# Performance work log

Hardware: AMD Instinct MI355X
Metric: run time of the kernel (lower is better)

Reference implementation:

```python
import jax, jax.numpy as jnp
import numpy as np

B, T, E, H = 8, 2048, 1024, 64

def setup_inputs() -> dict:
    key = jax.random.key(0)
    k1, k2, k3, k4 = jax.random.split(key, 4)
    x = jax.random.normal(k1, (B, T, E), dtype=jnp.float32)
    # Linear(E, H, bias=False) weights stored as [E, H] (x @ W)
    s = 1.0 / np.sqrt(E)
    Wk = jax.random.normal(k2, (E, H), dtype=jnp.float32) * s
    Wq = jax.random.normal(k3, (E, H), dtype=jnp.float32) * s
    Wv = jax.random.normal(k4, (E, H), dtype=jnp.float32) * s
    return {"x": x, "Wk": Wk, "Wq": Wq, "Wv": Wv}

def reference(x, Wk, Wq, Wv):
    _, t, e = x.shape
    k = jnp.einsum('bte,eh->bth', x, Wk)
    q = jnp.einsum('bte,eh->bth', x, Wq)
    v = jnp.einsum('bte,eh->bth', x, Wv)
    # NOTE: original scales by E**-0.5 (embedding dim), not head_size**-0.5
    wei = jnp.einsum('bqh,bkh->bqk', q, k) * (e ** -0.5)
    causal = jnp.tril(jnp.ones((t, t), dtype=bool))
    wei = jnp.where(causal, wei, -jnp.inf)
    wei = jax.nn.softmax(wei, axis=-1)
    out = jnp.einsum('bqk,bkh->bqh', wei, v)
    return out
```

## Files before the change

### kernel.cpp

```cpp
#include <hip/hip_runtime.h>

typedef unsigned short u16;
typedef unsigned int u32;
typedef __bf16 bf16x8 __attribute__((ext_vector_type(8)));
typedef __bf16 bf16x4 __attribute__((ext_vector_type(4)));
typedef float f32x4 __attribute__((ext_vector_type(4)));

constexpr int Bn = 8, Tn = 2048, En = 1024, Hn = 64;
constexpr int Mrows = Bn * Tn;
constexpr float CEXP = 0.03125f * 1.4426950408889634f;

__device__ __forceinline__ u16 f2bf(float f) {
  u32 u = __float_as_uint(f);
  return (u16)((u + 0x7fffu + ((u >> 16) & 1u)) >> 16);
}

__global__ __launch_bounds__(256) void wt_kernel(
    const float* __restrict__ Wk, const float* __restrict__ Wq,
    const float* __restrict__ Wv, u16* __restrict__ Wt2) {
  __shared__ float tile[64][68];
  const int mat = blockIdx.x >> 4;
  const int tk = blockIdx.x & 15;
  const float* W = (mat == 0) ? Wk : (mat == 1) ? Wq : Wv;
  const int t = threadIdx.x;
#pragma unroll
  for (int i = 0; i < 4; ++i) {
    const int f = t + i * 256;
    const int el = f >> 4;
    const int h4 = f & 15;
    float4 v = *(const float4*)(W + (size_t)(tk * 64 + el) * Hn + h4 * 4);
    tile[el][h4 * 4 + 0] = v.x;
    tile[el][h4 * 4 + 1] = v.y;
    tile[el][h4 * 4 + 2] = v.z;
    tile[el][h4 * 4 + 3] = v.w;
  }
  __syncthreads();
#pragma unroll
  for (int c2 = 0; c2 < 2; ++c2) {
    const int c = t * 2 + c2;
    const int fi = c >> 6;
    const int l = c & 63;
    const int ht = fi >> 1, kss = fi & 1;
    const int q = l >> 4, l16 = l & 15;
    __align__(16) u16 buf[8];
#pragma unroll
    for (int j = 0; j < 8; ++j)
      buf[j] = f2bf(tile[kss * 32 + q * 8 + j][ht * 16 + l16]);
    u16* dst = Wt2 + ((size_t)(tk * 12 + mat * 4 + ht) * 2 + kss) * 512 + l * 8;
    *(uint4*)dst = *(const uint4*)buf;
  }
}

__global__ __launch_bounds__(256, 2) void qkv_kernel(
    const float* __restrict__ x, const u16* __restrict__ Wt2,
    u16* __restrict__ Kb16, u16* __restrict__ Qb16, u16* __restrict__ Vt16) {
  constexpr int NR = 32, BK = 128, LDK = BK + 8;
  __shared__ u16 xs[NR * LDK];
  const int t = threadIdx.x;
  const int w = t >> 6, lane = t & 63;
  const int quad = lane >> 4, l16 = lane & 15;
  const int r0 = blockIdx.x * NR;

  const int srow = t >> 5;
  const int scol = (t & 31) * 4;
  const float* xp = x + (size_t)(r0 + srow) * En + scol;
  u16* xsw0 = xs + srow * LDK + scol;

  const u16* wA = Wt2 + (size_t)lane * 8;

  f32x4 acc[3][2];
#pragma unroll
  for (int i = 0; i < 3; ++i)
#pragma unroll
    for (int nt = 0; nt < 2; ++nt) acc[i][nt] = (f32x4){0.f, 0.f, 0.f, 0.f};

  bf16x8 af[2][12];

#define LOADA(P, K0)                                                            \
  do {                                                                          \
    const int tb_ = ((K0) >> 6) * 12;                                           \
    _Pragma("unroll") for (int ks_ = 0; ks_ < 4; ++ks_)                         \
        _Pragma("unroll") for (int i_ = 0; i_ < 3; ++i_) {                      \
      const int frag_ = (tb_ + (ks_ >> 1) * 12 + (3 * w + i_)) * 2 + (ks_ & 1); \
      af[P][ks_ * 3 + i_] = *(const bf16x8*)(wA + (size_t)frag_ * 512);         \
    }                                                                           \
  } while (0)

  float4 pre[4];
#pragma unroll
  for (int i = 0; i < 4; ++i) pre[i] = *(const float4*)(xp + i * 8 * En);
  LOADA(0, 0);

#pragma unroll
  for (int s = 0; s < 8; ++s) {
    const int k0 = s * BK;
    const int par = s & 1;
    __syncthreads();
#pragma unroll
    for (int i = 0; i < 4; ++i) {
      bf16x4 pk;
      pk[0] = (__bf16)pre[i].x; pk[1] = (__bf16)pre[i].y;
      pk[2] = (__bf16)pre[i].z; pk[3] = (__bf16)pre[i].w;
      *(bf16x4*)(xsw0 + i * 8 * LDK) = pk;
    }
    __syncthreads();
    if (s < 7) {
#pragma unroll
      for (int i = 0; i < 4; ++i)
        pre[i] = *(const float4*)(xp + k0 + BK + i * 8 * En);
      LOADA(par ^ 1, k0 + BK);
    }
#pragma unroll
    for (int ks = 0; ks < 4; ++ks) {
      bf16x8 b0 = *(const bf16x8*)(xs + l16 * LDK + ks * 32 + quad * 8);
      bf16x8 b1 = *(const bf16x8*)(xs + (16 + l16) * LDK + ks * 32 + quad * 8);
#pragma unroll
      for (int i = 0; i < 3; ++i) {
        acc[i][0] = __builtin_amdgcn_mfma_f32_16x16x32_bf16(af[par][ks * 3 + i], b0, acc[i][0], 0, 0, 0);
        acc[i][1] = __builtin_amdgcn_mfma_f32_16x16x32_bf16(af[par][ks * 3 + i], b1, acc[i][1], 0, 0, 0);
      }
    }
  }
#undef LOADA

#pragma unroll
  for (int i = 0; i < 3; ++i) {
    const int mt = 3 * w + i;
    const int mat = mt >> 2, ht = mt & 3;
#pragma unroll
    for (int nt = 0; nt < 2; ++nt) {
      const int row = r0 + nt * 16 + l16;
      f32x4 a = acc[i][nt];
      if (mat < 2) {
        u16* dst = ((mat == 0) ? Kb16 : Qb16) + (size_t)row * Hn + ht * 16 + quad * 4;
        uint2 pk;
        pk.x = (u32)f2bf(a[0]) | ((u32)f2bf(a[1]) << 16);
        pk.y = (u32)f2bf(a[2]) | ((u32)f2bf(a[3]) << 16);
        *(uint2*)dst = pk;
      } else {
        const int bb = row >> 11, tt = row & 2047;
        u16* base = Vt16 + ((size_t)bb * 64) * Tn + tt;
#pragma unroll
        for (int r = 0; r < 4; ++r)
          base[(size_t)(ht * 16 + quad * 4 + r) * Tn] = f2bf(a[r]);
      }
    }
  }
}

__global__ __launch_bounds__(256, 2) void attn_kernel(
    const u16* __restrict__ Qb16, const u16* __restrict__ Kb16,
    const u16* __restrict__ Vt16, float* __restrict__ out) {
  __shared__ u16 pt[2][4][2][16][40];
  __shared__ float l_sh[2][4][16];
  __shared__ float o_sh[2][4][16][68];

  const int idx = blockIdx.x;
  const int b = idx & 7;
  const int tq = 63 - (idx >> 3);
  const int w = threadIdx.x >> 6, lane = threadIdx.x & 63;
  const int quad = lane >> 4, l16 = lane & 15;
  const int qbase = tq * 32;
  const int limit = qbase + 32;
  const int ch = ((limit + 127) >> 7) << 5;
  const int lo = w * ch;
  const int hi = min(lo + ch, limit);
  const int qa_abs = qbase + l16;
  const int qb_abs = qbase + 16 + l16;

  const u16* Kp = Kb16 + (size_t)b * Tn * Hn;
  const u16* Vp = Vt16 + (size_t)b * 64 * Tn;

  const u16* qrowA = Qb16 + ((size_t)b * Tn + qa_abs) * Hn + quad * 8;
  const u16* qrowB = qrowA + (size_t)16 * Hn;
  const bf16x8 qa0 = *(const bf16x8*)(qrowA);
  const bf16x8 qa1 = *(const bf16x8*)(qrowA + 32);
  const bf16x8 qb0 = *(const bf16x8*)(qrowB);
  const bf16x8 qb1 = *(const bf16x8*)(qrowB + 32);

  f32x4 oA0 = {0.f, 0.f, 0.f, 0.f}, oA1 = oA0, oA2 = oA0, oA3 = oA0;
  f32x4 oB0 = oA0, oB1 = oA0, oB2 = oA0, oB3 = oA0;
  f32x4 laccA = oA0, laccB = oA0;

#pragma unroll 2
  for (int kb = lo; kb < hi; kb += 32) {
    const int par = (kb >> 5) & 1;
    const u16* krow0 = Kp + (size_t)(kb + l16) * Hn + quad * 8;
    const u16* krow1 = krow0 + (size_t)16 * Hn;
    const bf16x8 k0lo = *(const bf16x8*)(krow0);
    const bf16x8 k0hi = *(const bf16x8*)(krow0 + 32);
    const bf16x8 k1lo = *(const bf16x8*)(krow1);
    const bf16x8 k1hi = *(const bf16x8*)(krow1 + 32);

    const f32x4 z = {0.f, 0.f, 0.f, 0.f};
    f32x4 s0a = __builtin_amdgcn_mfma_f32_16x16x32_bf16(k0lo, qa0, z, 0, 0, 0);
    s0a = __builtin_amdgcn_mfma_f32_16x16x32_bf16(k0hi, qa1, s0a, 0, 0, 0);
    f32x4 s1a = __builtin_amdgcn_mfma_f32_16x16x32_bf16(k1lo, qa0, z, 0, 0, 0);
    s1a = __builtin_amdgcn_mfma_f32_16x16x32_bf16(k1hi, qa1, s1a, 0, 0, 0);
    f32x4 s0b = __builtin_amdgcn_mfma_f32_16x16x32_bf16(k0lo, qb0, z, 0, 0, 0);
    s0b = __builtin_amdgcn_mfma_f32_16x16x32_bf16(k0hi, qb1, s0b, 0, 0, 0);
    f32x4 s1b = __builtin_amdgcn_mfma_f32_16x16x32_bf16(k1lo, qb0, z, 0, 0, 0);
    s1b = __builtin_amdgcn_mfma_f32_16x16x32_bf16(k1hi, qb1, s1b, 0, 0, 0);

    if (kb + 15 > qbase) {
#pragma unroll
      for (int r = 0; r < 4; ++r)
        if (kb + quad * 4 + r > qa_abs) s0a[r] = -3.0e38f;
    }
    if (kb + 31 > qbase) {
#pragma unroll
      for (int r = 0; r < 4; ++r)
        if (kb + 16 + quad * 4 + r > qa_abs) s1a[r] = -3.0e38f;
    }
    if (kb + 15 > qbase + 16) {
#pragma unroll
      for (int r = 0; r < 4; ++r)
        if (kb + quad * 4 + r > qb_abs) s0b[r] = -3.0e38f;
    }
    if (kb + 31 > qbase + 16) {
#pragma unroll
      for (int r = 0; r < 4; ++r)
        if (kb + 16 + quad * 4 + r > qb_abs) s1b[r] = -3.0e38f;
    }

    f32x4 pa0, pa1, pb0v, pb1v;
#pragma unroll
    for (int r = 0; r < 4; ++r) {
      pa0[r] = __builtin_amdgcn_exp2f(s0a[r] * CEXP);
      pa1[r] = __builtin_amdgcn_exp2f(s1a[r] * CEXP);
      pb0v[r] = __builtin_amdgcn_exp2f(s0b[r] * CEXP);
      pb1v[r] = __builtin_amdgcn_exp2f(s1b[r] * CEXP);
    }
    laccA += pa0;
    laccA += pa1;
    laccB += pb0v;
    laccB += pb1v;

    {
      bf16x4 wa0, wa1, wb0, wb1;
      wa0[0] = (__bf16)pa0[0]; wa0[1] = (__bf16)pa0[1];
      wa0[2] = (__bf16)pa0[2]; wa0[3] = (__bf16)pa0[3];
      wa1[0] = (__bf16)pa1[0]; wa1[1] = (__bf16)pa1[1];
      wa1[2] = (__bf16)pa1[2]; wa1[3] = (__bf16)pa1[3];
      wb0[0] = (__bf16)pb0v[0]; wb0[1] = (__bf16)pb0v[1];
      wb0[2] = (__bf16)pb0v[2]; wb0[3] = (__bf16)pb0v[3];
      wb1[0] = (__bf16)pb1v[0]; wb1[1] = (__bf16)pb1v[1];
      wb1[2] = (__bf16)pb1v[2]; wb1[3] = (__bf16)pb1v[3];
      *(bf16x4*)&pt[par][w][0][l16][quad * 4] = wa0;
      *(bf16x4*)&pt[par][w][0][l16][16 + quad * 4] = wa1;
      *(bf16x4*)&pt[par][w][1][l16][quad * 4] = wb0;
      *(bf16x4*)&pt[par][w][1][l16][16 + quad * 4] = wb1;
    }
    const bf16x8 pba = *(const bf16x8*)&pt[par][w][0][l16][quad * 8];
    const bf16x8 pbb = *(const bf16x8*)&pt[par][w][1][l16][quad * 8];

    const u16* vrow = Vp + (size_t)l16 * Tn + kb + quad * 8;
    const bf16x8 v0 = *(const bf16x8*)(vrow);
    const bf16x8 v1 = *(const bf16x8*)(vrow + (size_t)16 * Tn);
    const bf16x8 v2 = *(const bf16x8*)(vrow + (size_t)32 * Tn);
    const bf16x8 v3 = *(const bf16x8*)(vrow + (size_t)48 * Tn);

    oA0 = __builtin_amdgcn_mfma_f32_16x16x32_bf16(v0, pba, oA0, 0, 0, 0);
    oA1 = __builtin_amdgcn_mfma_f32_16x16x32_bf16(v1, pba, oA1, 0, 0, 0);
    oA2 = __builtin_amdgcn_mfma_f32_16x16x32_bf16(v2, pba, oA2, 0, 0, 0);
    oA3 = __builtin_amdgcn_mfma_f32_16x16x32_bf16(v3, pba, oA3, 0, 0, 0);
    oB0 = __builtin_amdgcn_mfma_f32_16x16x32_bf16(v0, pbb, oB0, 0, 0, 0);
    oB1 = __builtin_amdgcn_mfma_f32_16x16x32_bf16(v1, pbb, oB1, 0, 0, 0);
    oB2 = __builtin_amdgcn_mfma_f32_16x16x32_bf16(v2, pbb, oB2, 0, 0, 0);
    oB3 = __builtin_amdgcn_mfma_f32_16x16x32_bf16(v3, pbb, oB3, 0, 0, 0);
  }

  float la = (laccA[0] + laccA[1]) + (laccA[2] + laccA[3]);
  la += __shfl_xor(la, 16);
  la += __shfl_xor(la, 32);
  float lb = (laccB[0] + laccB[1]) + (laccB[2] + laccB[3]);
  lb += __shfl_xor(lb, 16);
  lb += __shfl_xor(lb, 32);
  if (quad == 0) {
    l_sh[0][w][l16] = la;
    l_sh[1][w][l16] = lb;
  }
  *(f32x4*)&o_sh[0][w][l16][0 * 16 + quad * 4] = oA0;
  *(f32x4*)&o_sh[0][w][l16][1 * 16 + quad * 4] = oA1;
  *(f32x4*)&o_sh[0][w][l16][2 * 16 + quad * 4] = oA2;
  *(f32x4*)&o_sh[0][w][l16][3 * 16 + quad * 4] = oA3;
  *(f32x4*)&o_sh[1][w][l16][0 * 16 + quad * 4] = oB0;
  *(f32x4*)&o_sh[1][w][l16][1 * 16 + quad * 4] = oB1;
  *(f32x4*)&o_sh[1][w][l16][2 * 16 + quad * 4] = oB2;
  *(f32x4*)&o_sh[1][w][l16][3 * 16 + quad * 4] = oB3;
  __syncthreads();

  const int qq = threadIdx.x >> 4, dq = threadIdx.x & 15;
#pragma unroll
  for (int tl = 0; tl < 2; ++tl) {
    float lg = 0.f;
    f32x4 acc = {0.f, 0.f, 0.f, 0.f};
#pragma unroll
    for (int ww = 0; ww < 4; ++ww) {
      lg += l_sh[tl][ww][qq];
      acc += *(const f32x4*)&o_sh[tl][ww][qq][dq * 4];
    }
    acc *= (1.f / lg);
    *(f32x4*)(out + ((size_t)b * Tn + qbase + tl * 16 + qq) * Hn + dq * 4) = acc;
  }
}

extern "C" void kernel_launch(void* const* d_in, const int* in_sizes, int n_in,
                              void* d_out, int out_size, void* d_ws, size_t ws_size,
                              hipStream_t stream) {
  const void* x = nullptr;
  const void* Ws[3] = {nullptr, nullptr, nullptr};
  int wj = 0;
  for (int i = 0; i < n_in; ++i) {
    if (in_sizes[i] == Bn * Tn * En) x = d_in[i];
    else if (wj < 3) Ws[wj++] = d_in[i];
  }
  const float* Wk = (const float*)Ws[0];
  const float* Wq = (const float*)Ws[1];
  const float* Wv = (const float*)Ws[2];

  u16* Kb16 = (u16*)d_ws;
  u16* Qb16 = Kb16 + (size_t)Mrows * Hn;
  u16* Vt16 = Qb16 + (size_t)Mrows * Hn;
  u16* Wt2  = Vt16 + (size_t)Mrows * Hn;

  wt_kernel<<<48, 256, 0, stream>>>(Wk, Wq, Wv, Wt2);
  qkv_kernel<<<Mrows / 32, 256, 0, stream>>>((const float*)x, Wt2, Kb16, Qb16, Vt16);
  attn_kernel<<<Bn * (Tn / 32), 256, 0, stream>>>(Qb16, Kb16, Vt16, (float*)d_out);
}
```

Before: 134.6 us.

## Split attention key range across eight waves per block with two-phase LDS reduction

New measurement: 134.8 us. Within noise of the previous version (+0.1%).

```diff
diff --git a/kernel.cpp b/kernel.cpp
--- a/kernel.cpp
+++ b/kernel.cpp
@@ -148,12 +148,14 @@
   }
 }
 
-__global__ __launch_bounds__(256, 2) void attn_kernel(
+__global__ __launch_bounds__(512, 4) void attn_kernel(
     const u16* __restrict__ Qb16, const u16* __restrict__ Kb16,
     const u16* __restrict__ Vt16, float* __restrict__ out) {
-  __shared__ u16 pt[2][4][2][16][40];
-  __shared__ float l_sh[2][4][16];
-  __shared__ float o_sh[2][4][16][68];
+  __shared__ __align__(16) char arena[34816];
+  __shared__ float l_sh[8][32];
+
+  u16* ptb = (u16*)arena;
+  float* osb = (float*)arena;
 
   const int idx = blockIdx.x;
   const int b = idx & 7;
@@ -162,7 +164,7 @@
   const int quad = lane >> 4, l16 = lane & 15;
   const int qbase = tq * 32;
   const int limit = qbase + 32;
-  const int ch = ((limit + 127) >> 7) << 5;
+  const int ch = ((limit + 255) >> 8) << 5;
   const int lo = w * ch;
   const int hi = min(lo + ch, limit);
   const int qa_abs = qbase + l16;
@@ -178,13 +180,14 @@
   const bf16x8 qb0 = *(const bf16x8*)(qrowB);
   const bf16x8 qb1 = *(const bf16x8*)(qrowB + 32);
 
+  u16* ptw = ptb + (size_t)w * (2 * 16 * 40);
+
   f32x4 oA0 = {0.f, 0.f, 0.f, 0.f}, oA1 = oA0, oA2 = oA0, oA3 = oA0;
   f32x4 oB0 = oA0, oB1 = oA0, oB2 = oA0, oB3 = oA0;
   f32x4 laccA = oA0, laccB = oA0;
 
 #pragma unroll 2
   for (int kb = lo; kb < hi; kb += 32) {
-    const int par = (kb >> 5) & 1;
     const u16* krow0 = Kp + (size_t)(kb + l16) * Hn + quad * 8;
     const u16* krow1 = krow0 + (size_t)16 * Hn;
     const bf16x8 k0lo = *(const bf16x8*)(krow0);
@@ -246,13 +249,13 @@
       wb0[2] = (__bf16)pb0v[2]; wb0[3] = (__bf16)pb0v[3];
       wb1[0] = (__bf16)pb1v[0]; wb1[1] = (__bf16)pb1v[1];
       wb1[2] = (__bf16)pb1v[2]; wb1[3] = (__bf16)pb1v[3];
-      *(bf16x4*)&pt[par][w][0][l16][quad * 4] = wa0;
-      *(bf16x4*)&pt[par][w][0][l16][16 + quad * 4] = wa1;
-      *(bf16x4*)&pt[par][w][1][l16][quad * 4] = wb0;
-      *(bf16x4*)&pt[par][w][1][l16][16 + quad * 4] = wb1;
-    }
-    const bf16x8 pba = *(const bf16x8*)&pt[par][w][0][l16][quad * 8];
-    const bf16x8 pbb = *(const bf16x8*)&pt[par][w][1][l16][quad * 8];
+      *(bf16x4*)&ptw[l16 * 40 + quad * 4] = wa0;
+      *(bf16x4*)&ptw[l16 * 40 + 16 + quad * 4] = wa1;
+      *(bf16x4*)&ptw[640 + l16 * 40 + quad * 4] = wb0;
+      *(bf16x4*)&ptw[640 + l16 * 40 + 16 + quad * 4] = wb1;
+    }
+    const bf16x8 pba = *(const bf16x8*)&ptw[l16 * 40 + quad * 8];
+    const bf16x8 pbb = *(const bf16x8*)&ptw[640 + l16 * 40 + quad * 8];
 
     const u16* vrow = Vp + (size_t)l16 * Tn + kb + quad * 8;
     const bf16x8 v0 = *(const bf16x8*)(vrow);
@@ -277,32 +280,55 @@
   lb += __shfl_xor(lb, 16);
   lb += __shfl_xor(lb, 32);
   if (quad == 0) {
-    l_sh[0][w][l16] = la;
-    l_sh[1][w][l16] = lb;
-  }
-  *(f32x4*)&o_sh[0][w][l16][0 * 16 + quad * 4] = oA0;
-  *(f32x4*)&o_sh[0][w][l16][1 * 16 + quad * 4] = oA1;
-  *(f32x4*)&o_sh[0][w][l16][2 * 16 + quad * 4] = oA2;
-  *(f32x4*)&o_sh[0][w][l16][3 * 16 + quad * 4] = oA3;
-  *(f32x4*)&o_sh[1][w][l16][0 * 16 + quad * 4] = oB0;
-  *(f32x4*)&o_sh[1][w][l16][1 * 16 + quad * 4] = oB1;
-  *(f32x4*)&o_sh[1][w][l16][2 * 16 + quad * 4] = oB2;
-  *(f32x4*)&o_sh[1][w][l16][3 * 16 + quad * 4] = oB3;
+    l_sh[w][l16] = la;
+    l_sh[w][16 + l16] = lb;
+  }
+  __syncthreads();
+
+  if (w < 4) {
+    float* o0 = osb + ((size_t)w * 32 + l16) * 68;
+    *(f32x4*)(o0 + 0 * 16 + quad * 4) = oA0;
+    *(f32x4*)(o0 + 1 * 16 + quad * 4) = oA1;
+    *(f32x4*)(o0 + 2 * 16 + quad * 4) = oA2;
+    *(f32x4*)(o0 + 3 * 16 + quad * 4) = oA3;
+    float* o1 = osb + ((size_t)w * 32 + 16 + l16) * 68;
+    *(f32x4*)(o1 + 0 * 16 + quad * 4) = oB0;
+    *(f32x4*)(o1 + 1 * 16 + quad * 4) = oB1;
+    *(f32x4*)(o1 + 2 * 16 + quad * 4) = oB2;
+    *(f32x4*)(o1 + 3 * 16 + quad * 4) = oB3;
+  }
   __syncthreads();
 
   const int qq = threadIdx.x >> 4, dq = threadIdx.x & 15;
-#pragma unroll
-  for (int tl = 0; tl < 2; ++tl) {
-    float lg = 0.f;
-    f32x4 acc = {0.f, 0.f, 0.f, 0.f};
-#pragma unroll
-    for (int ww = 0; ww < 4; ++ww) {
-      lg += l_sh[tl][ww][qq];
-      acc += *(const f32x4*)&o_sh[tl][ww][qq][dq * 4];
-    }
-    acc *= (1.f / lg);
-    *(f32x4*)(out + ((size_t)b * Tn + qbase + tl * 16 + qq) * Hn + dq * 4) = acc;
-  }
+  f32x4 part = {0.f, 0.f, 0.f, 0.f};
+#pragma unroll
+  for (int ww = 0; ww < 4; ++ww)
+    part += *(const f32x4*)&osb[((size_t)ww * 32 + qq) * 68 + dq * 4];
+  __syncthreads();
+
+  if (w >= 4) {
+    float* o0 = osb + ((size_t)(w - 4) * 32 + l16) * 68;
+    *(f32x4*)(o0 + 0 * 16 + quad * 4) = oA0;
+    *(f32x4*)(o0 + 1 * 16 + quad * 4) = oA1;
+    *(f32x4*)(o0 + 2 * 16 + quad * 4) = oA2;
+    *(f32x4*)(o0 + 3 * 16 + quad * 4) = oA3;
+    float* o1 = osb + ((size_t)(w - 4) * 32 + 16 + l16) * 68;
+    *(f32x4*)(o1 + 0 * 16 + quad * 4) = oB0;
+    *(f32x4*)(o1 + 1 * 16 + quad * 4) = oB1;
+    *(f32x4*)(o1 + 2 * 16 + quad * 4) = oB2;
+    *(f32x4*)(o1 + 3 * 16 + quad * 4) = oB3;
+  }
+  __syncthreads();
+
+#pragma unroll
+  for (int ww = 0; ww < 4; ++ww)
+    part += *(const f32x4*)&osb[((size_t)ww * 32 + qq) * 68 + dq * 4];
+
+  float lg = 0.f;
+#pragma unroll
+  for (int ww = 0; ww < 8; ++ww) lg += l_sh[ww][qq];
+  part *= (1.f / lg);
+  *(f32x4*)(out + ((size_t)b * Tn + qbase + qq) * Hn + dq * 4) = part;
 }
 
 extern "C" void kernel_launch(void* const* d_in, const int* in_sizes, int n_in,
@@ -326,5 +352,5 @@
 
   wt_kernel<<<48, 256, 0, stream>>>(Wk, Wq, Wv, Wt2);
   qkv_kernel<<<Mrows / 32, 256, 0, stream>>>((const float*)x, Wt2, Kb16, Qb16, Vt16);
-  attn_kernel<<<Bn * (Tn / 32), 256, 0, stream>>>(Qb16, Kb16, Vt16, (float*)d_out);
-}
+  attn_kernel<<<Bn * (Tn / 32), 512, 0, stream>>>(Qb16, Kb16, Vt16, (float*)d_out);
+}
```
